# Kernel tuning notes

Hardware: AMD Instinct MI355X
Metric: run time of the kernel (lower is better)

Reference implementation:

```python
import jax, jax.numpy as jnp
import numpy as np
import math

N_QUBITS = 8
N_QLAYERS = 2
NUM_HEADS = 2


def run_circuit(x, weights):
    """Simulate PennyLane circuit: AngleEmbedding(RX) + BasicEntanglerLayers(RX + CNOT ring),
    measure <Z_i> on every wire.  x: (T, n) real angles, weights: (L, n) real angles.
    Returns (T, n) expectation values."""
    T, n = x.shape
    L = weights.shape[0]
    # AngleEmbedding: product state prod_q RX(x_q)|0> = [cos(x/2), -i sin(x/2)]
    half = 0.5 * x
    amps = jnp.stack([jnp.cos(half).astype(jnp.complex64),
                      (-1j) * jnp.sin(half).astype(jnp.complex64)], axis=-1)  # (T, n, 2)
    state = amps[:, 0, :]  # (T, 2)
    for q in range(1, n):
        state = (state[:, :, None] * amps[:, q][:, None, :]).reshape(T, -1)
    state = state.reshape((T,) + (2,) * n)  # qubit 0 = axis 1 (most significant)

    for l in range(L):
        cl = jnp.cos(0.5 * weights[l]).astype(jnp.complex64)
        sl = jnp.sin(0.5 * weights[l]).astype(jnp.complex64)
        # RX(weights[l, q]) on each wire (shared angle across tokens)
        for q in range(n):
            s0 = jnp.take(state, 0, axis=1 + q)
            s1 = jnp.take(state, 1, axis=1 + q)
            n0 = cl[q] * s0 - 1j * sl[q] * s1
            n1 = -1j * sl[q] * s0 + cl[q] * s1
            state = jnp.stack([n0, n1], axis=1 + q)
        # CNOT ring: control q -> target (q+1) % n
        for q in range(n):
            ctrl, tgt = q, (q + 1) % n
            s0 = jnp.take(state, 0, axis=1 + ctrl)
            s1 = jnp.take(state, 1, axis=1 + ctrl)
            t_axis = 1 + tgt - (1 if tgt > ctrl else 0)  # target axis after removing ctrl axis
            s1 = jnp.flip(s1, axis=t_axis)
            state = jnp.stack([s0, s1], axis=1 + ctrl)

    probs = (state.real ** 2 + state.imag ** 2).reshape(T, 2 ** n)
    # <Z_q> = sum_idx probs[idx] * (1 - 2*bit_q(idx)); qubit 0 is MSB
    idx = np.arange(2 ** n)
    bits = (idx[None, :] >> np.arange(n - 1, -1, -1)[:, None]) & 1  # (n, 2^n)
    signs = jnp.asarray(1 - 2 * bits, dtype=probs.dtype)
    return probs @ signs.T  # (T, n)


def setup_inputs() -> dict:
    key = jax.random.key(0)
    kx, kq, kk, kv, kc = jax.random.split(key, 5)
    B, S, E = 32, 1024, N_QUBITS
    two_pi = 2.0 * math.pi
    return {
        "x": jax.random.normal(kx, (B, S, E), dtype=jnp.float32),
        "wq": jax.random.uniform(kq, (N_QLAYERS, N_QUBITS), dtype=jnp.float32) * two_pi,
        "wk": jax.random.uniform(kk, (N_QLAYERS, N_QUBITS), dtype=jnp.float32) * two_pi,
        "wv": jax.random.uniform(kv, (N_QLAYERS, N_QUBITS), dtype=jnp.float32) * two_pi,
        "wc": jax.random.uniform(kc, (N_QLAYERS, N_QUBITS), dtype=jnp.float32) * two_pi,
    }


def reference(x, wq, wk, wv, wc):
    B, S, E = x.shape
    H = NUM_HEADS
    d_k = E // H
    tok = x.reshape(B * S, E)
    Q = run_circuit(tok, wq).reshape(B, S, H, d_k).transpose(0, 2, 1, 3)  # (B,H,S,d)
    K = run_circuit(tok, wk).reshape(B, S, H, d_k).transpose(0, 2, 1, 3)
    V = run_circuit(tok, wv).reshape(B, S, H, d_k).transpose(0, 2, 1, 3)
    scores = jnp.einsum('bhqd,bhkd->bhqk', Q, K) / jnp.sqrt(jnp.asarray(d_k, x.dtype))
    attn = jax.nn.softmax(scores, axis=-1)  # dropout is identity in eval mode
    ctx = jnp.einsum('bhqk,bhkd->bhqd', attn, V)  # (B,H,S,d)
    ctx = ctx.transpose(0, 2, 1, 3).reshape(B, S, E)
    out = run_circuit(ctx.reshape(B * S, E), wc).reshape(B, S, E)
    return out
```

## Files before the change

kernel.cpp:

```cpp
#include <hip/hip_runtime.h>

#define TT 32768
#define S_LEN 1024

__device__ __align__(16) float g_Q[TT * 8];
__device__ __align__(16) float g_K[TT * 8];
__device__ __align__(16) float g_V[TT * 8];
__device__ __align__(16) float4 gp_acc[4 * 64 * 1024];
__device__ float gp_den[4 * 64 * 1024];
__device__ float g_coef[4][8][128];

struct PTerm { unsigned ymask, zonly, tmask; float sgn; };
struct OTab { PTerm t[128]; int n; unsigned amask; };

constexpr unsigned conjZring(unsigned a) {
    for (int q = 7; q >= 0; --q) {
        const int c = q, tt = (q + 1) & 7;
        if ((a >> tt) & 1u) a ^= (1u << c);
    }
    return a;
}
constexpr unsigned conjXring(unsigned b) {
    for (int q = 7; q >= 0; --q) {
        const int c = q, tt = (q + 1) & 7;
        if ((b >> c) & 1u) b ^= (1u << tt);
    }
    return b;
}
constexpr int popc8(unsigned v) { int n = 0; for (int i = 0; i < 8; ++i) n += (v >> i) & 1; return n; }

constexpr OTab build_tab(int i) {
    OTab o{};
    o.n = 0;
    const unsigned a1 = conjZring(1u << i);
    o.amask = a1;
    const unsigned a3 = conjZring(a1);
    unsigned T = a1;
    while (true) {
        const unsigned b3 = conjXring(T);
        if (!(b3 & ~a3)) {
            const int k = popc8(T) + popc8(b3);
            const int idx = (k & 1) ? 100000 : o.n;
            o.t[idx].ymask = b3;
            o.t[idx].zonly = a3 & ~b3;
            o.t[idx].tmask = T;
            o.t[idx].sgn = ((k >> 1) & 1) ? -1.f : 1.f;
            o.n++;
        }
        if (T == 0) break;
        T = (T - 1) & a1;
    }
    return o;
}

constexpr OTab g_tab[8] = {build_tab(0), build_tab(1), build_tab(2), build_tab(3),
                           build_tab(4), build_tab(5), build_tab(6), build_tab(7)};
static_assert(g_tab[0].n >= 1 && g_tab[0].n <= 128, "term count");
static_assert(g_tab[7].n >= 1 && g_tab[7].n <= 128, "term count");

template <int I>
__device__ __forceinline__ void coef_one(const float s1[8], const float c1[8], float* dst)
{
    constexpr OTab tb = g_tab[I];
#pragma unroll
    for (int k = 0; k < tb.n; ++k) {
        float c = tb.t[k].sgn;
#pragma unroll
        for (int q = 0; q < 8; ++q) {
            if ((tb.t[k].tmask >> q) & 1) c *= s1[q];
            else if ((tb.amask >> q) & 1) c *= c1[q];
        }
        dst[k] = c;
    }
}

__global__ __launch_bounds__(64) void precoef(
    const float* __restrict__ wq, const float* __restrict__ wk,
    const float* __restrict__ wv, const float* __restrict__ wc)
{
    int tid = threadIdx.x;
    if (tid >= 32) return;
    int set = tid >> 3, i = tid & 7;
    const float* w = (set == 0) ? wq : (set == 1) ? wk : (set == 2) ? wv : wc;
    float s1[8], c1[8];
#pragma unroll
    for (int q = 0; q < 8; ++q) __sincosf(w[8 + q], &s1[q], &c1[q]);
    float* dst = &g_coef[set][i][0];
    switch (i) {
        case 0: coef_one<0>(s1, c1, dst); break;
        case 1: coef_one<1>(s1, c1, dst); break;
        case 2: coef_one<2>(s1, c1, dst); break;
        case 3: coef_one<3>(s1, c1, dst); break;
        case 4: coef_one<4>(s1, c1, dst); break;
        case 5: coef_one<5>(s1, c1, dst); break;
        case 6: coef_one<6>(s1, c1, dst); break;
        case 7: coef_one<7>(s1, c1, dst); break;
    }
}

template <int I>
__device__ __forceinline__ float eval_out(const float cs[8], const float sn[8],
                                          const float* __restrict__ coefI)
{
    constexpr OTab tb = g_tab[I];
    float acc = 0.f;
#pragma unroll
    for (int k = 0; k < tb.n; ++k) {
        float p = coefI[k];
#pragma unroll
        for (int q = 0; q < 8; ++q) {
            if ((tb.t[k].ymask >> q) & 1) p *= sn[q];
            else if ((tb.t[k].zonly >> q) & 1) p *= cs[q];
        }
        acc += p;
    }
    return acc;
}

__device__ __forceinline__ void eval_all(const float th[8],
                                         const float (*__restrict__ coef)[128],
                                         float ev[8])
{
    float cs[8], sn[8];
#pragma unroll
    for (int q = 0; q < 8; ++q) __sincosf(th[q], &sn[q], &cs[q]);
    ev[0] = eval_out<0>(cs, sn, coef[0]);
    ev[1] = eval_out<1>(cs, sn, coef[1]);
    ev[2] = eval_out<2>(cs, sn, coef[2]);
    ev[3] = eval_out<3>(cs, sn, coef[3]);
    ev[4] = eval_out<4>(cs, sn, coef[4]);
    ev[5] = eval_out<5>(cs, sn, coef[5]);
    ev[6] = eval_out<6>(cs, sn, coef[6]);
    ev[7] = eval_out<7>(cs, sn, coef[7]);
}

#define QSCALE 0.72134752044448170368f

__global__ __launch_bounds__(256) void qkv_pauli(
    const float* __restrict__ x, const float* __restrict__ wq,
    const float* __restrict__ wk, const float* __restrict__ wv)
{
    int t = blockIdx.x * 256 + threadIdx.x;
    int set = blockIdx.y;
    const float* w = (set == 0) ? wq : (set == 1) ? wk : wv;
    float* out = (set == 0) ? g_Q : (set == 1) ? g_K : g_V;
    float4 xa = ((const float4*)x)[t * 2];
    float4 xb = ((const float4*)x)[t * 2 + 1];
    float th[8] = {xa.x + w[0], xa.y + w[1], xa.z + w[2], xa.w + w[3],
                   xb.x + w[4], xb.y + w[5], xb.z + w[6], xb.w + w[7]};
    float ev[8];
    eval_all(th, g_coef[set], ev);
    float sc = (set == 0) ? QSCALE : 1.f;
#pragma unroll
    for (int i = 0; i < 8; ++i) ev[i] *= sc;
    ((float4*)out)[t * 2]     = make_float4(ev[0], ev[1], ev[2], ev[3]);
    ((float4*)out)[t * 2 + 1] = make_float4(ev[4], ev[5], ev[6], ev[7]);
}

__global__ __launch_bounds__(256) void attn_part()
{
    __shared__ float4 Ks[256];
    __shared__ float4 Vs[256];
    int bh = blockIdx.x, qc = blockIdx.y, kc = blockIdx.z;
    int b = bh >> 1, h = bh & 1;
    int tid = threadIdx.x;
    int q = qc * 256 + tid;
    const float* Qp = g_Q + ((size_t)b * S_LEN + q) * 8 + h * 4;
    float4 qv = *(const float4*)Qp;
    size_t row = (size_t)b * S_LEN + kc * 256 + tid;
    Ks[tid] = *(const float4*)(g_K + row * 8 + h * 4);
    Vs[tid] = *(const float4*)(g_V + row * 8 + h * 4);
    __syncthreads();
    float den = 0.f;
    float4 acc = make_float4(0.f, 0.f, 0.f, 0.f);
    for (int k = 0; k < 256; ++k) {
        float4 kk = Ks[k];
        float s = qv.x * kk.x + qv.y * kk.y + qv.z * kk.z + qv.w * kk.w;
        float e = exp2f(s);
        den += e;
        float4 vv = Vs[k];
        acc.x += e * vv.x; acc.y += e * vv.y; acc.z += e * vv.z; acc.w += e * vv.w;
    }
    int idx = kc * 65536 + bh * 1024 + q;
    gp_acc[idx] = acc;
    gp_den[idx] = den;
}

__global__ __launch_bounds__(256) void outc_pauli(
    const float* __restrict__ wc, float* __restrict__ out)
{
    int t = blockIdx.x * 256 + threadIdx.x;
    int b = t >> 10, s = t & 1023;
    float th[8];
#pragma unroll
    for (int h = 0; h < 2; ++h) {
        float4 A = make_float4(0.f, 0.f, 0.f, 0.f);
        float D = 0.f;
#pragma unroll
        for (int kc = 0; kc < 4; ++kc) {
            int idx = kc * 65536 + (b * 2 + h) * 1024 + s;
            float4 a = gp_acc[idx];
            A.x += a.x; A.y += a.y; A.z += a.z; A.w += a.w;
            D += gp_den[idx];
        }
        float inv = 1.f / D;
        th[h * 4 + 0] = A.x * inv + wc[h * 4 + 0];
        th[h * 4 + 1] = A.y * inv + wc[h * 4 + 1];
        th[h * 4 + 2] = A.z * inv + wc[h * 4 + 2];
        th[h * 4 + 3] = A.w * inv + wc[h * 4 + 3];
    }
    float ev[8];
    eval_all(th, g_coef[3], ev);
    ((float4*)out)[t * 2]     = make_float4(ev[0], ev[1], ev[2], ev[3]);
    ((float4*)out)[t * 2 + 1] = make_float4(ev[4], ev[5], ev[6], ev[7]);
}

extern "C" void kernel_launch(void* const* d_in, const int* in_sizes, int n_in,
                              void* d_out, int out_size, void* d_ws, size_t ws_size,
                              hipStream_t stream)
{
    const float* x  = (const float*)d_in[0];
    const float* wq = (const float*)d_in[1];
    const float* wk = (const float*)d_in[2];
    const float* wv = (const float*)d_in[3];
    const float* wc = (const float*)d_in[4];

    precoef<<<1, 64, 0, stream>>>(wq, wk, wv, wc);
    qkv_pauli<<<dim3(TT / 256, 3), 256, 0, stream>>>(x, wq, wk, wv);
    attn_part<<<dim3(64, 4, 4), 256, 0, stream>>>();
    outc_pauli<<<TT / 256, 256, 0, stream>>>(wc, (float*)d_out);
}
```

Baseline: 48.49 us.

## Register-block four queries per thread in attention partials, split keys eightfold

Each attention block now covers all 1024 queries of a batch-head, four per thread, against a 128-key chunk. Keys are split into 8 chunks instead of 4 query by 4 key tiles. Every K/V value read from LDS is reused across four queries, which cuts LDS traffic per FLOP and adds independent exp and FMA chains. In exchange the partial-sum buffers are twice as large, so the output kernel reads 8 partials per token, and half the threads sit idle while K/V is loaded.

```diff
diff --git a/kernel.cpp b/kernel.cpp
--- a/kernel.cpp
+++ b/kernel.cpp
@@ -2,12 +2,13 @@
 
 #define TT 32768
 #define S_LEN 1024
+#define KC 8
 
 __device__ __align__(16) float g_Q[TT * 8];
 __device__ __align__(16) float g_K[TT * 8];
 __device__ __align__(16) float g_V[TT * 8];
-__device__ __align__(16) float4 gp_acc[4 * 64 * 1024];
-__device__ float gp_den[4 * 64 * 1024];
+__device__ __align__(16) float4 gp_acc[KC * 64 * 1024];
+__device__ float gp_den[KC * 64 * 1024];
 __device__ float g_coef[4][8][128];
 
 struct PTerm { unsigned ymask, zonly, tmask; float sgn; };
@@ -159,31 +160,50 @@
 
 __global__ __launch_bounds__(256) void attn_part()
 {
-    __shared__ float4 Ks[256];
-    __shared__ float4 Vs[256];
-    int bh = blockIdx.x, qc = blockIdx.y, kc = blockIdx.z;
+    __shared__ float4 Ks[128];
+    __shared__ float4 Vs[128];
+    int bh = blockIdx.x, kc = blockIdx.y;
     int b = bh >> 1, h = bh & 1;
     int tid = threadIdx.x;
-    int q = qc * 256 + tid;
-    const float* Qp = g_Q + ((size_t)b * S_LEN + q) * 8 + h * 4;
-    float4 qv = *(const float4*)Qp;
-    size_t row = (size_t)b * S_LEN + kc * 256 + tid;
-    Ks[tid] = *(const float4*)(g_K + row * 8 + h * 4);
-    Vs[tid] = *(const float4*)(g_V + row * 8 + h * 4);
+
+    const float* Qb = g_Q + (size_t)b * S_LEN * 8 + h * 4;
+    float4 qv0 = *(const float4*)(Qb + (size_t)(tid        ) * 8);
+    float4 qv1 = *(const float4*)(Qb + (size_t)(tid + 256  ) * 8);
+    float4 qv2 = *(const float4*)(Qb + (size_t)(tid + 512  ) * 8);
+    float4 qv3 = *(const float4*)(Qb + (size_t)(tid + 768  ) * 8);
+
+    if (tid < 128) {
+        size_t row = (size_t)b * S_LEN + kc * 128 + tid;
+        Ks[tid] = *(const float4*)(g_K + row * 8 + h * 4);
+        Vs[tid] = *(const float4*)(g_V + row * 8 + h * 4);
+    }
     __syncthreads();
-    float den = 0.f;
-    float4 acc = make_float4(0.f, 0.f, 0.f, 0.f);
-    for (int k = 0; k < 256; ++k) {
+
+    float den0 = 0.f, den1 = 0.f, den2 = 0.f, den3 = 0.f;
+    float4 ac0 = make_float4(0.f, 0.f, 0.f, 0.f);
+    float4 ac1 = make_float4(0.f, 0.f, 0.f, 0.f);
+    float4 ac2 = make_float4(0.f, 0.f, 0.f, 0.f);
+    float4 ac3 = make_float4(0.f, 0.f, 0.f, 0.f);
+#pragma unroll 4
+    for (int k = 0; k < 128; ++k) {
         float4 kk = Ks[k];
-        float s = qv.x * kk.x + qv.y * kk.y + qv.z * kk.z + qv.w * kk.w;
-        float e = exp2f(s);
-        den += e;
         float4 vv = Vs[k];
-        acc.x += e * vv.x; acc.y += e * vv.y; acc.z += e * vv.z; acc.w += e * vv.w;
-    }
-    int idx = kc * 65536 + bh * 1024 + q;
-    gp_acc[idx] = acc;
-    gp_den[idx] = den;
+        float s0 = qv0.x * kk.x + qv0.y * kk.y + qv0.z * kk.z + qv0.w * kk.w;
+        float s1 = qv1.x * kk.x + qv1.y * kk.y + qv1.z * kk.z + qv1.w * kk.w;
+        float s2 = qv2.x * kk.x + qv2.y * kk.y + qv2.z * kk.z + qv2.w * kk.w;
+        float s3 = qv3.x * kk.x + qv3.y * kk.y + qv3.z * kk.z + qv3.w * kk.w;
+        float e0 = exp2f(s0), e1 = exp2f(s1), e2 = exp2f(s2), e3 = exp2f(s3);
+        den0 += e0; den1 += e1; den2 += e2; den3 += e3;
+        ac0.x += e0 * vv.x; ac0.y += e0 * vv.y; ac0.z += e0 * vv.z; ac0.w += e0 * vv.w;
+        ac1.x += e1 * vv.x; ac1.y += e1 * vv.y; ac1.z += e1 * vv.z; ac1.w += e1 * vv.w;
+        ac2.x += e2 * vv.x; ac2.y += e2 * vv.y; ac2.z += e2 * vv.z; ac2.w += e2 * vv.w;
+        ac3.x += e3 * vv.x; ac3.y += e3 * vv.y; ac3.z += e3 * vv.z; ac3.w += e3 * vv.w;
+    }
+    int base = kc * 65536 + bh * 1024 + tid;
+    gp_acc[base]       = ac0;  gp_den[base]       = den0;
+    gp_acc[base + 256] = ac1;  gp_den[base + 256] = den1;
+    gp_acc[base + 512] = ac2;  gp_den[base + 512] = den2;
+    gp_acc[base + 768] = ac3;  gp_den[base + 768] = den3;
 }
 
 __global__ __launch_bounds__(256) void outc_pauli(
@@ -197,7 +217,7 @@
         float4 A = make_float4(0.f, 0.f, 0.f, 0.f);
         float D = 0.f;
 #pragma unroll
-        for (int kc = 0; kc < 4; ++kc) {
+        for (int kc = 0; kc < KC; ++kc) {
             int idx = kc * 65536 + (b * 2 + h) * 1024 + s;
             float4 a = gp_acc[idx];
             A.x += a.x; A.y += a.y; A.z += a.z; A.w += a.w;
@@ -227,6 +247,6 @@
 
     precoef<<<1, 64, 0, stream>>>(wq, wk, wv, wc);
     qkv_pauli<<<dim3(TT / 256, 3), 256, 0, stream>>>(x, wq, wk, wv);
-    attn_part<<<dim3(64, 4, 4), 256, 0, stream>>>();
+    attn_part<<<dim3(64, KC), 256, 0, stream>>>();
     outc_pauli<<<TT / 256, 256, 0, stream>>>(wc, (float*)d_out);
 }
```

New measurement: 52.27 us. +7.8%, slower.
